# Kernel optimization log

Measured on AMD Instinct MI355X. Metric: run time of the kernel, lower is better.

The kernel has to match this reference:

```python
import jax, jax.numpy as jnp
import numpy as np

B, S, F = 2048, 1024, 64  # batch, n_support, num_features

def setup_inputs() -> dict:
    key = jax.random.key(0)
    k1, k2, k3, k4 = jax.random.split(key, 4)
    X = jax.random.normal(k1, (B, F), dtype=jnp.float32)
    support = jax.random.normal(k2, (S, F), dtype=jnp.float32)
    W = jax.random.normal(k3, (1, S), dtype=jnp.float32) * (1.0 / np.sqrt(S))
    b = jax.random.normal(k4, (1,), dtype=jnp.float32)
    return {"X": X, "support": support, "W": W, "b": b}

def reference(X, support, W, b):
    # Quantum kernel: product states from RX rotations are tensor products of
    # [cos(t/2), -i sin(t/2)] per qubit; the overlap factorizes exactly as
    # <psi(a)|psi(b)> = prod_f cos((a_f - b_f)/2), hence
    # K[i,j] = |overlap|^2 = prod_f cos^2((X[i,f] - support[j,f]) / 2).
    diff = X[:, None, :] - support[None, :, :]          # [B, S, F]
    c = jnp.cos(diff * 0.5)
    K = jnp.prod(c * c, axis=-1)                        # [B, S]
    # Linear head: K @ W^T + b, then squeeze(-1) -> [B]
    return K @ W[0] + b[0]
```

## Files before the change

### kernel.cpp

```cpp
#include <hip/hip_runtime.h>
#include <math.h>

#define B_ 2048
#define S_ 1024
#define F_ 64

typedef _Float16 half2_t __attribute__((ext_vector_type(2)));

__global__ __launch_bounds__(256, 4) void qkr_fused(
    const float* __restrict__ X, const float* __restrict__ Sup,
    const float* __restrict__ W, const float* __restrict__ b,
    float* __restrict__ out)
{
    __shared__ half2_t sX[64][64];
    __shared__ half2_t sS[64][64];

    const int t  = threadIdx.x;
    const int i0 = blockIdx.x * 64;
    const int j0 = blockIdx.y * 64;

    const int r  = t >> 2;
    const int fs = (t & 3) << 4;
    #pragma unroll
    for (int q = 0; q < 4; ++q) {
        const float4 v = *(const float4*)&X[(size_t)(i0 + r) * F_ + fs + q * 4];
        float c, s;
        __sincosf(v.x, &s, &c); sX[fs + q*4 + 0][r] = (half2_t){(_Float16)(0.5f*c), (_Float16)(0.5f*s)};
        __sincosf(v.y, &s, &c); sX[fs + q*4 + 1][r] = (half2_t){(_Float16)(0.5f*c), (_Float16)(0.5f*s)};
        __sincosf(v.z, &s, &c); sX[fs + q*4 + 2][r] = (half2_t){(_Float16)(0.5f*c), (_Float16)(0.5f*s)};
        __sincosf(v.w, &s, &c); sX[fs + q*4 + 3][r] = (half2_t){(_Float16)(0.5f*c), (_Float16)(0.5f*s)};
    }
    #pragma unroll
    for (int q = 0; q < 4; ++q) {
        const float4 v = *(const float4*)&Sup[(size_t)(j0 + r) * F_ + fs + q * 4];
        float c, s;
        __sincosf(v.x, &s, &c); sS[fs + q*4 + 0][r] = (half2_t){(_Float16)c, (_Float16)s};
        __sincosf(v.y, &s, &c); sS[fs + q*4 + 1][r] = (half2_t){(_Float16)c, (_Float16)s};
        __sincosf(v.z, &s, &c); sS[fs + q*4 + 2][r] = (half2_t){(_Float16)c, (_Float16)s};
        __sincosf(v.w, &s, &c); sS[fs + q*4 + 3][r] = (half2_t){(_Float16)c, (_Float16)s};
    }
    __syncthreads();

    const int tx = t & 15;
    const int ty = t >> 4;

    float p[4][4];
    #pragma unroll
    for (int a = 0; a < 4; ++a)
        #pragma unroll
        for (int c = 0; c < 4; ++c) p[a][c] = 1.0f;

    #pragma unroll 4
    for (int f = 0; f < 64; ++f) {
        union { float4 v; half2_t h[4]; } ux, us;
        ux.v = *(const float4*)&sX[f][ty * 4];
        us.v = *(const float4*)&sS[f][tx * 4];
        #pragma unroll
        for (int a = 0; a < 4; ++a) {
            #pragma unroll
            for (int c = 0; c < 4; ++c) {
#if __has_builtin(__builtin_amdgcn_fdot2)
                const float term = __builtin_amdgcn_fdot2(ux.h[a], us.h[c], 0.5f, false);
#else
                const float term = 0.5f + (float)ux.h[a].x * (float)us.h[c].x
                                        + (float)ux.h[a].y * (float)us.h[c].y;
#endif
                p[a][c] *= term;
            }
        }
    }

    const float4 w4 = *(const float4*)&W[j0 + tx * 4];
    const float wj[4] = {w4.x, w4.y, w4.z, w4.w};
    const float bv = (blockIdx.y == 0) ? b[0] : 0.0f;
    #pragma unroll
    for (int a = 0; a < 4; ++a) {
        float acc = p[a][0] * wj[0];
        acc = fmaf(p[a][1], wj[1], acc);
        acc = fmaf(p[a][2], wj[2], acc);
        acc = fmaf(p[a][3], wj[3], acc);
        acc += __shfl_xor(acc, 1);
        acc += __shfl_xor(acc, 2);
        acc += __shfl_xor(acc, 4);
        acc += __shfl_xor(acc, 8);
        if (tx == 0) atomicAdd(&out[i0 + ty * 4 + a], acc + bv);
    }
}

extern "C" void kernel_launch(void* const* d_in, const int* in_sizes, int n_in,
                              void* d_out, int out_size, void* d_ws, size_t ws_size,
                              hipStream_t stream) {
    const float* X   = (const float*)d_in[0];
    const float* Sup = (const float*)d_in[1];
    const float* W   = (const float*)d_in[2];
    const float* b   = (const float*)d_in[3];
    float* out = (float*)d_out;
    (void)d_ws; (void)ws_size;

    qkr_fused<<<dim3(32, 16), dim3(256), 0, stream>>>(X, Sup, W, b, out);
}
```

Measured before the change: 70.18 us.

## Precompute half-precision sin/cos features in a separate prep kernel

Splits the fused kernel into a prep kernel and a main kernel. The prep kernel computes sincos of X and support once, packs the results as fp16 pairs in transposed feature-major layout, and writes them to workspace. The main kernel then fills shared memory with plain vector copies, so each tile no longer recomputes the same sincos values. In exchange it adds a second launch and a round-trip of the precomputed data through global memory.

```diff
diff --git a/kernel.cpp b/kernel.cpp
--- a/kernel.cpp
+++ b/kernel.cpp
@@ -7,8 +7,35 @@
 
 typedef _Float16 half2_t __attribute__((ext_vector_type(2)));
 
-__global__ __launch_bounds__(256, 4) void qkr_fused(
+__global__ __launch_bounds__(256) void qkr_prep(
     const float* __restrict__ X, const float* __restrict__ Sup,
+    half2_t* __restrict__ hXT, half2_t* __restrict__ hST)
+{
+    const int t = threadIdx.x;
+    int bid = blockIdx.x;
+    float c, s;
+    if (bid < 128) {
+        const int i  = ((bid & 7) << 8) + t;
+        const int f4 = bid >> 3;
+        const float4 v = *(const float4*)&X[(size_t)i * F_ + f4 * 4];
+        __sincosf(v.x, &s, &c); hXT[(size_t)(f4*4+0)*B_ + i] = (half2_t){(_Float16)(0.5f*c), (_Float16)(0.5f*s)};
+        __sincosf(v.y, &s, &c); hXT[(size_t)(f4*4+1)*B_ + i] = (half2_t){(_Float16)(0.5f*c), (_Float16)(0.5f*s)};
+        __sincosf(v.z, &s, &c); hXT[(size_t)(f4*4+2)*B_ + i] = (half2_t){(_Float16)(0.5f*c), (_Float16)(0.5f*s)};
+        __sincosf(v.w, &s, &c); hXT[(size_t)(f4*4+3)*B_ + i] = (half2_t){(_Float16)(0.5f*c), (_Float16)(0.5f*s)};
+    } else {
+        bid -= 128;
+        const int j  = ((bid & 3) << 8) + t;
+        const int f4 = bid >> 2;
+        const float4 v = *(const float4*)&Sup[(size_t)j * F_ + f4 * 4];
+        __sincosf(v.x, &s, &c); hST[(size_t)(f4*4+0)*S_ + j] = (half2_t){(_Float16)c, (_Float16)s};
+        __sincosf(v.y, &s, &c); hST[(size_t)(f4*4+1)*S_ + j] = (half2_t){(_Float16)c, (_Float16)s};
+        __sincosf(v.z, &s, &c); hST[(size_t)(f4*4+2)*S_ + j] = (half2_t){(_Float16)c, (_Float16)s};
+        __sincosf(v.w, &s, &c); hST[(size_t)(f4*4+3)*S_ + j] = (half2_t){(_Float16)c, (_Float16)s};
+    }
+}
+
+__global__ __launch_bounds__(256, 4) void qkr_main(
+    const half2_t* __restrict__ hXT, const half2_t* __restrict__ hST,
     const float* __restrict__ W, const float* __restrict__ b,
     float* __restrict__ out)
 {
@@ -19,25 +46,19 @@
     const int i0 = blockIdx.x * 64;
     const int j0 = blockIdx.y * 64;
 
-    const int r  = t >> 2;
-    const int fs = (t & 3) << 4;
-    #pragma unroll
-    for (int q = 0; q < 4; ++q) {
-        const float4 v = *(const float4*)&X[(size_t)(i0 + r) * F_ + fs + q * 4];
-        float c, s;
-        __sincosf(v.x, &s, &c); sX[fs + q*4 + 0][r] = (half2_t){(_Float16)(0.5f*c), (_Float16)(0.5f*s)};
-        __sincosf(v.y, &s, &c); sX[fs + q*4 + 1][r] = (half2_t){(_Float16)(0.5f*c), (_Float16)(0.5f*s)};
-        __sincosf(v.z, &s, &c); sX[fs + q*4 + 2][r] = (half2_t){(_Float16)(0.5f*c), (_Float16)(0.5f*s)};
-        __sincosf(v.w, &s, &c); sX[fs + q*4 + 3][r] = (half2_t){(_Float16)(0.5f*c), (_Float16)(0.5f*s)};
-    }
-    #pragma unroll
-    for (int q = 0; q < 4; ++q) {
-        const float4 v = *(const float4*)&Sup[(size_t)(j0 + r) * F_ + fs + q * 4];
-        float c, s;
-        __sincosf(v.x, &s, &c); sS[fs + q*4 + 0][r] = (half2_t){(_Float16)c, (_Float16)s};
-        __sincosf(v.y, &s, &c); sS[fs + q*4 + 1][r] = (half2_t){(_Float16)c, (_Float16)s};
-        __sincosf(v.z, &s, &c); sS[fs + q*4 + 2][r] = (half2_t){(_Float16)c, (_Float16)s};
-        __sincosf(v.w, &s, &c); sS[fs + q*4 + 3][r] = (half2_t){(_Float16)c, (_Float16)s};
+    {
+        const float4* gX = (const float4*)hXT;
+        const float4* gS = (const float4*)hST;
+        float4* lX = (float4*)sX;
+        float4* lS = (float4*)sS;
+        #pragma unroll
+        for (int q = 0; q < 4; ++q) {
+            const int e = q * 256 + t;
+            const int f = e >> 4;
+            const int p = e & 15;
+            lX[e] = gX[(size_t)f * (B_/4) + (i0 >> 2) + p];
+            lS[e] = gS[(size_t)f * (S_/4) + (j0 >> 2) + p];
+        }
     }
     __syncthreads();
 
@@ -95,7 +116,11 @@
     const float* W   = (const float*)d_in[2];
     const float* b   = (const float*)d_in[3];
     float* out = (float*)d_out;
-    (void)d_ws; (void)ws_size;
 
-    qkr_fused<<<dim3(32, 16), dim3(256), 0, stream>>>(X, Sup, W, b, out);
+    half2_t* hXT = (half2_t*)d_ws;
+    half2_t* hST = (half2_t*)((char*)d_ws + (size_t)F_ * B_ * 4);
+    (void)ws_size; (void)in_sizes; (void)n_in; (void)out_size;
+
+    qkr_prep<<<dim3(192), dim3(256), 0, stream>>>(X, Sup, hXT, hST);
+    qkr_main<<<dim3(32, 16), dim3(256), 0, stream>>>(hXT, hST, W, b, out);
 }
```

Result: slower. 71.87 us (+2.4%).
